# Kernel optimization log

Measured on AMD Instinct MI355X. Metric: run time of the kernel, lower is better.

Reference implementation:

```python
import jax, jax.numpy as jnp
import numpy as np

B, H, P, D = 32, 8, 16, 32
OUT_DIM = 32
GROUPS = 64
NUM_F = 8
N = H * P * D                 # 4096 (self.num)
PHO = P * H * OUT_DIM         # 4096


def setup_inputs() -> dict:
    key = jax.random.key(0)
    ks = jax.random.split(key, 10)
    return {
        "q": jax.random.normal(ks[0], (B, H, P, D), dtype=jnp.float32),
        "k": jax.random.normal(ks[1], (B, H, P, D), dtype=jnp.float32),
        "grid": jnp.arange(NUM_F, dtype=jnp.float32) + 1.0,
        "base_weight_q": jax.random.uniform(ks[2], (PHO, N), dtype=jnp.float32),
        "base_weight_k": jax.random.uniform(ks[3], (PHO, N), dtype=jnp.float32),
        "coef_q": jax.random.uniform(ks[4], (GROUPS, 1, NUM_F), dtype=jnp.float32),
        "coef_k": jax.random.uniform(ks[5], (GROUPS, 1, NUM_F), dtype=jnp.float32),
        # grouped 1x1 conv == num_f independent [PHO, N] matmuls (only conv_layer_q is used in forward)
        "conv_wq": jax.random.normal(ks[6], (NUM_F, PHO, N), dtype=jnp.float32) * 0.01,
        "conv_bq": jax.random.normal(ks[7], (NUM_F, PHO), dtype=jnp.float32) * 0.01,
        "scale_sp": jnp.ones((PHO,), dtype=jnp.float32),
    }


def reference(q, k, grid, base_weight_q, base_weight_k, coef_q, coef_k, conv_wq, conv_bq, scale_sp):
    b, h, p, d = q.shape
    n = h * p * d
    nf = grid.shape[0]
    gs = n // coef_q.shape[0]               # group_size
    out_dim = base_weight_q.shape[0] // (p * h)

    qf = q.reshape(b, n)
    kf = k.reshape(b, n)

    base_q = jax.nn.silu(qf) @ base_weight_q.T          # [B, PHO]
    base_k = jax.nn.silu(kf) @ base_weight_k.T

    # per-feature coef: feature i in group i//gs, scaled per frequency f -> [F, N]
    ce_q = jnp.repeat(coef_q[:, 0, :], gs, axis=0).T
    ce_k = jnp.repeat(coef_k[:, 0, :], gs, axis=0).T

    sq = jnp.sin(grid[None, :, None] * qf[:, None, :]) * ce_q[None]   # [B, F, N]
    sk = jnp.sin(grid[None, :, None] * kf[:, None, :]) * ce_k[None]

    # grouped conv1d (kernel 1, groups=num_f): per-frequency matmul; original uses conv_layer_q for both
    fq = jnp.einsum('bfn,fon->bfo', sq, conv_wq) + conv_bq[None]      # [B, F, PHO]
    fq = fq.sum(axis=1) * scale_sp
    fk = jnp.einsum('bfn,fon->bfo', sk, conv_wq) + conv_bq[None]
    fk = fk.sum(axis=1) * scale_sp

    y = (fq * scale_sp + base_q) + (fk * scale_sp + base_k)
    y = y.reshape(b, h, p, out_dim)
    return jax.nn.softmax(y, axis=-1)
```

## Files before the change

### kernel.cpp

```cpp
#include <hip/hip_runtime.h>
#include <math.h>

#define N_TOT 4096
#define PHO_T 4096
#define KTOT  40960
#define NS    2560

typedef __attribute__((ext_vector_type(8)))  short short8v;
typedef __attribute__((ext_vector_type(16))) float f32x16;

#define GLD16(src, dst) __builtin_amdgcn_global_load_lds(                      \
    (const __attribute__((address_space(1))) void*)(src),                      \
    (__attribute__((address_space(3))) void*)(dst), 16, 0, 0)

__device__ __forceinline__ void split1(float x, short& h, short& l) {
    unsigned u  = __builtin_bit_cast(unsigned, x);
    unsigned hu = (u + 0x7FFFu + ((u >> 16) & 1u)) & 0xFFFF0000u;
    h = (short)(hu >> 16);
    float r = x - __builtin_bit_cast(float, hu);
    unsigned ur = __builtin_bit_cast(unsigned, r);
    l = (short)((ur + 0x7FFFu + ((ur >> 16) & 1u)) >> 16);
}

__global__ void act_kernel(const float* __restrict__ q,
                           const float* __restrict__ kx,
                           const float* __restrict__ grid_,
                           const float* __restrict__ coefq,
                           const float* __restrict__ coefk,
                           short* __restrict__ Af)
{
    const int t = blockIdx.x * 256 + threadIdx.x;
    const int S = t >> 6;
    const int l = t & 63;
    const int b = l & 31;
    const int k0 = S * 16 + (l >> 5) * 8;

    float v[8];
    if (k0 < 8192) {
        const float* src = (k0 < 4096) ? (q  + (size_t)b * N_TOT + k0)
                                       : (kx + (size_t)b * N_TOT + (k0 - 4096));
#pragma unroll
        for (int j = 0; j < 8; ++j) {
            const float x = src[j];
            v[j] = x / (1.f + __expf(-x));
        }
    } else {
        const int f  = (k0 - 8192) >> 12;
        const int n0 = (k0 - 8192) & 4095;
        const int g  = n0 >> 6;
        const float gf  = grid_[f];
        const float cq_ = coefq[g * 8 + f];
        const float ck_ = coefk[g * 8 + f];
        const float* qp = q  + (size_t)b * N_TOT + n0;
        const float* kp = kx + (size_t)b * N_TOT + n0;
#pragma unroll
        for (int j = 0; j < 8; ++j)
            v[j] = __sinf(gf * qp[j]) * cq_ + __sinf(gf * kp[j]) * ck_;
    }

    short8v hi, lo;
#pragma unroll
    for (int j = 0; j < 8; ++j) { short h, lw; split1(v[j], h, lw); hi[j] = h; lo[j] = lw; }
    *(short8v*)&Af[((size_t)(S * 2 + 0) * 64 + l) * 8] = hi;
    *(short8v*)&Af[((size_t)(S * 2 + 1) * 64 + l) * 8] = lo;
}

__global__ void init_kernel(const float* __restrict__ cb,
                            const float* __restrict__ ssp,
                            float* __restrict__ ypre)
{
    const int t = blockIdx.x * 256 + threadIdx.x;
    const int o = t & 4095;
    const float s = ssp[o];
    float acc = 0.f;
#pragma unroll
    for (int f = 0; f < 8; ++f) acc += cb[f * PHO_T + o];
    ypre[t] = 2.f * s * s * acc;
}

#define OBK  256
#define KC   32
#define KSUP 1280
#define NCH  (KSUP / KC)

__global__ __launch_bounds__(256) void gemm_kernel(
    const float* __restrict__ bwq, const float* __restrict__ bwk,
    const float* __restrict__ cw,  const short* __restrict__ Af,
    const float* __restrict__ ssp, float* __restrict__ ypre)
{
    __shared__ float Wl[2][OBK * KC];

    const int t  = threadIdx.x;
    const int ks = blockIdx.x >> 4;
    const int ob = blockIdx.x & 15;
    const int o_base = ob * OBK;
    const int k_base = ks * KSUP;

    const int w  = t >> 6;
    const int l  = t & 63;
    const int srow  = l >> 3;
    const int sslot = (l & 7) ^ (srow & 7);

    f32x16 accU0, accU1, accS0, accS1;
#pragma unroll
    for (int i = 0; i < 16; ++i) {
        accU0[i] = 0.f; accU1[i] = 0.f; accS0[i] = 0.f; accS1[i] = 0.f;
    }

    auto wptr = [&](int kg) -> const float* {
        if (kg < 4096)  return bwq + kg;
        if (kg < 8192)  return bwk + (kg - 4096);
        const int f    = (kg - 8192) >> 12;
        const int noff = (kg - 8192) & 4095;
        return cw + (size_t)f * (size_t)PHO_T * N_TOT + noff;
    };

    auto stage = [&](int kg, int buf) {
        const float* Wp = wptr(kg);
#pragma unroll
        for (int i = 0; i < 8; ++i) {
            const int row = w * 64 + i * 8 + srow;
            const float* src = Wp + (size_t)(o_base + row) * N_TOT + sslot * 4;
            GLD16(src, &Wl[buf][(w * 64 + i * 8) * KC]);
        }
    };

    const int rkey = l & 7;
    const int row0 = w * 64 + (l & 31);
    const int j0b  = (l >> 5) * 2;

    auto compute = [&](int kg, int cur, const short8v& ah0, const short8v& al0,
                       const short8v& ah1, const short8v& al1) {
        const bool sc = (kg >= 8192);
#pragma unroll
        for (int s = 0; s < 2; ++s) {
            const short8v& ah = s ? ah1 : ah0;
            const short8v& al = s ? al1 : al0;
            const int j0 = s * 4 + j0b;

            auto tileop = [&](int nt, f32x16& acc) {
                const float* rp = &Wl[cur][(row0 + nt * 32) * KC];
                const float4 wa = *(const float4*)&rp[((j0    ) ^ rkey) * 4];
                const float4 wb = *(const float4*)&rp[((j0 + 1) ^ rkey) * 4];
                short8v bh, bl;
                {
                    short h, lw;
                    split1(wa.x, h, lw); bh[0] = h; bl[0] = lw;
                    split1(wa.y, h, lw); bh[1] = h; bl[1] = lw;
                    split1(wa.z, h, lw); bh[2] = h; bl[2] = lw;
                    split1(wa.w, h, lw); bh[3] = h; bl[3] = lw;
                    split1(wb.x, h, lw); bh[4] = h; bl[4] = lw;
                    split1(wb.y, h, lw); bh[5] = h; bl[5] = lw;
                    split1(wb.z, h, lw); bh[6] = h; bl[6] = lw;
                    split1(wb.w, h, lw); bh[7] = h; bl[7] = lw;
                }
                acc = __builtin_amdgcn_mfma_f32_32x32x16_bf16(ah, bh, acc, 0, 0, 0);
                acc = __builtin_amdgcn_mfma_f32_32x32x16_bf16(ah, bl, acc, 0, 0, 0);
                acc = __builtin_amdgcn_mfma_f32_32x32x16_bf16(al, bh, acc, 0, 0, 0);
            };
            if (sc) { tileop(0, accS0); tileop(1, accS1); }
            else    { tileop(0, accU0); tileop(1, accU1); }
        }
    };

    stage(k_base, 0);

    short8v ah0, al0, ah1, al1;
    for (int c = 0; c < NCH - 1; ++c) {
        const int cur = c & 1;
        const int kg  = k_base + c * KC;
        const size_t Sg = (size_t)(kg >> 4);
        ah0 = *(const short8v*)&Af[(((Sg    ) * 2 + 0) * 64 + l) * 8];
        al0 = *(const short8v*)&Af[(((Sg    ) * 2 + 1) * 64 + l) * 8];
        ah1 = *(const short8v*)&Af[(((Sg + 1) * 2 + 0) * 64 + l) * 8];
        al1 = *(const short8v*)&Af[(((Sg + 1) * 2 + 1) * 64 + l) * 8];
        asm volatile("" ::: "memory");
        stage(kg + KC, cur ^ 1);
        asm volatile("s_waitcnt vmcnt(8)" ::: "memory");
        __builtin_amdgcn_sched_barrier(0);
        compute(kg, cur, ah0, al0, ah1, al1);
    }
    {
        const int c   = NCH - 1;
        const int kg  = k_base + c * KC;
        const size_t Sg = (size_t)(kg >> 4);
        ah0 = *(const short8v*)&Af[(((Sg    ) * 2 + 0) * 64 + l) * 8];
        al0 = *(const short8v*)&Af[(((Sg    ) * 2 + 1) * 64 + l) * 8];
        ah1 = *(const short8v*)&Af[(((Sg + 1) * 2 + 0) * 64 + l) * 8];
        al1 = *(const short8v*)&Af[(((Sg + 1) * 2 + 1) * 64 + l) * 8];
        asm volatile("s_waitcnt vmcnt(0)" ::: "memory");
        __builtin_amdgcn_sched_barrier(0);
        compute(kg, c & 1, ah0, al0, ah1, al1);
    }

    const int o0 = o_base + w * 64 + (l & 31);
    const int o1 = o0 + 32;
    const float x0 = ssp[o0], x1 = ssp[o1];
    const float s0 = x0 * x0, s1 = x1 * x1;
    const int bh4 = 4 * (l >> 5);
#pragma unroll
    for (int r = 0; r < 16; ++r) {
        const int b = (r & 3) + 8 * (r >> 2) + bh4;
        atomicAdd(&ypre[(size_t)b * PHO_T + o0], accU0[r] + accS0[r] * s0);
        atomicAdd(&ypre[(size_t)b * PHO_T + o1], accU1[r] + accS1[r] * s1);
    }
}

__global__ void softmax_kernel(const float* __restrict__ yp,
                               float* __restrict__ out)
{
    const int t  = threadIdx.x;
    const int r  = blockIdx.x * 8 + (t >> 5);
    const int od = t & 31;
    const float v = yp[(size_t)r * 32 + od];
    float m = v;
#pragma unroll
    for (int s = 16; s > 0; s >>= 1) m = fmaxf(m, __shfl_xor(m, s, 32));
    const float e = __expf(v - m);
    float sum = e;
#pragma unroll
    for (int s = 16; s > 0; s >>= 1) sum += __shfl_xor(sum, s, 32);
    out[(size_t)r * 32 + od] = e / sum;
}

extern "C" void kernel_launch(void* const* d_in, const int* in_sizes, int n_in,
                              void* d_out, int out_size, void* d_ws, size_t ws_size,
                              hipStream_t stream)
{
    const float* q    = (const float*)d_in[0];
    const float* k    = (const float*)d_in[1];
    const float* grid = (const float*)d_in[2];
    const float* bwq  = (const float*)d_in[3];
    const float* bwk  = (const float*)d_in[4];
    const float* cq   = (const float*)d_in[5];
    const float* ck   = (const float*)d_in[6];
    const float* cw   = (const float*)d_in[7];
    const float* cb   = (const float*)d_in[8];
    const float* ssp  = (const float*)d_in[9];
    float* out = (float*)d_out;

    short* Af   = (short*)d_ws;
    float* ypre = (float*)((char*)d_ws + (size_t)NS * 2 * 64 * 16);

    act_kernel<<<640, 256, 0, stream>>>(q, k, grid, cq, ck, Af);
    init_kernel<<<512, 256, 0, stream>>>(cb, ssp, ypre);
    gemm_kernel<<<512, 256, 0, stream>>>(bwq, bwk, cw, Af, ssp, ypre);
    softmax_kernel<<<512, 256, 0, stream>>>(ypre, out);
}
```

Measured before the change: 142.6 us.

## Halve GEMM output tile, double grid, remap blocks, fuse init into act kernel

The output block width in the split-K GEMM drops from 256 to 128 rows, so the grid doubles from 512 to 1024 blocks and each wave keeps one accumulator pair instead of two. Block indices are remapped so that consecutive blocks share an output block while covering different K slices. The bias/init kernel is folded into the activation kernel to remove one launch. The aim is more parallelism over the 256 CUs and lower register pressure. The cost is that each A fragment is reused across fewer MFMA tiles, A-fragment global loads double, and twice as many LDS stages are issued per FLOP.

```diff
diff --git a/kernel.cpp b/kernel.cpp
--- a/kernel.cpp
+++ b/kernel.cpp
@@ -27,7 +27,10 @@
                            const float* __restrict__ grid_,
                            const float* __restrict__ coefq,
                            const float* __restrict__ coefk,
-                           short* __restrict__ Af)
+                           const float* __restrict__ cb,
+                           const float* __restrict__ ssp,
+                           short* __restrict__ Af,
+                           float* __restrict__ ypre)
 {
     const int t = blockIdx.x * 256 + threadIdx.x;
     const int S = t >> 6;
@@ -63,22 +66,18 @@
     for (int j = 0; j < 8; ++j) { short h, lw; split1(v[j], h, lw); hi[j] = h; lo[j] = lw; }
     *(short8v*)&Af[((size_t)(S * 2 + 0) * 64 + l) * 8] = hi;
     *(short8v*)&Af[((size_t)(S * 2 + 1) * 64 + l) * 8] = lo;
-}
-
-__global__ void init_kernel(const float* __restrict__ cb,
-                            const float* __restrict__ ssp,
-                            float* __restrict__ ypre)
-{
-    const int t = blockIdx.x * 256 + threadIdx.x;
-    const int o = t & 4095;
-    const float s = ssp[o];
-    float acc = 0.f;
-#pragma unroll
-    for (int f = 0; f < 8; ++f) acc += cb[f * PHO_T + o];
-    ypre[t] = 2.f * s * s * acc;
-}
-
-#define OBK  256
+
+    if (t < 32 * PHO_T) {
+        const int o = t & 4095;
+        const float s = ssp[o];
+        float acc = 0.f;
+#pragma unroll
+        for (int f = 0; f < 8; ++f) acc += cb[f * PHO_T + o];
+        ypre[t] = 2.f * s * s * acc;
+    }
+}
+
+#define OBK  128
 #define KC   32
 #define KSUP 1280
 #define NCH  (KSUP / KC)
@@ -90,9 +89,10 @@
 {
     __shared__ float Wl[2][OBK * KC];
 
-    const int t  = threadIdx.x;
-    const int ks = blockIdx.x >> 4;
-    const int ob = blockIdx.x & 15;
+    const int t   = threadIdx.x;
+    const int bid = blockIdx.x;
+    const int ks  = ((bid >> 3) & 3) * 8 + (bid & 7);
+    const int ob  = bid >> 5;
     const int o_base = ob * OBK;
     const int k_base = ks * KSUP;
 
@@ -101,11 +101,9 @@
     const int srow  = l >> 3;
     const int sslot = (l & 7) ^ (srow & 7);
 
-    f32x16 accU0, accU1, accS0, accS1;
-#pragma unroll
-    for (int i = 0; i < 16; ++i) {
-        accU0[i] = 0.f; accU1[i] = 0.f; accS0[i] = 0.f; accS1[i] = 0.f;
-    }
+    f32x16 accU, accS;
+#pragma unroll
+    for (int i = 0; i < 16; ++i) { accU[i] = 0.f; accS[i] = 0.f; }
 
     auto wptr = [&](int kg) -> const float* {
         if (kg < 4096)  return bwq + kg;
@@ -118,15 +116,15 @@
     auto stage = [&](int kg, int buf) {
         const float* Wp = wptr(kg);
 #pragma unroll
-        for (int i = 0; i < 8; ++i) {
-            const int row = w * 64 + i * 8 + srow;
+        for (int i = 0; i < 4; ++i) {
+            const int row = w * 32 + i * 8 + srow;
             const float* src = Wp + (size_t)(o_base + row) * N_TOT + sslot * 4;
-            GLD16(src, &Wl[buf][(w * 64 + i * 8) * KC]);
+            GLD16(src, &Wl[buf][(w * 32 + i * 8) * KC]);
         }
     };
 
     const int rkey = l & 7;
-    const int row0 = w * 64 + (l & 31);
+    const int row0 = w * 32 + (l & 31);
     const int j0b  = (l >> 5) * 2;
 
     auto compute = [&](int kg, int cur, const short8v& ah0, const short8v& al0,
@@ -138,28 +136,25 @@
             const short8v& al = s ? al1 : al0;
             const int j0 = s * 4 + j0b;
 
-            auto tileop = [&](int nt, f32x16& acc) {
-                const float* rp = &Wl[cur][(row0 + nt * 32) * KC];
-                const float4 wa = *(const float4*)&rp[((j0    ) ^ rkey) * 4];
-                const float4 wb = *(const float4*)&rp[((j0 + 1) ^ rkey) * 4];
-                short8v bh, bl;
-                {
-                    short h, lw;
-                    split1(wa.x, h, lw); bh[0] = h; bl[0] = lw;
-                    split1(wa.y, h, lw); bh[1] = h; bl[1] = lw;
-                    split1(wa.z, h, lw); bh[2] = h; bl[2] = lw;
-                    split1(wa.w, h, lw); bh[3] = h; bl[3] = lw;
-                    split1(wb.x, h, lw); bh[4] = h; bl[4] = lw;
-                    split1(wb.y, h, lw); bh[5] = h; bl[5] = lw;
-                    split1(wb.z, h, lw); bh[6] = h; bl[6] = lw;
-                    split1(wb.w, h, lw); bh[7] = h; bl[7] = lw;
-                }
-                acc = __builtin_amdgcn_mfma_f32_32x32x16_bf16(ah, bh, acc, 0, 0, 0);
-                acc = __builtin_amdgcn_mfma_f32_32x32x16_bf16(ah, bl, acc, 0, 0, 0);
-                acc = __builtin_amdgcn_mfma_f32_32x32x16_bf16(al, bh, acc, 0, 0, 0);
-            };
-            if (sc) { tileop(0, accS0); tileop(1, accS1); }
-            else    { tileop(0, accU0); tileop(1, accU1); }
+            const float* rp = &Wl[cur][row0 * KC];
+            const float4 wa = *(const float4*)&rp[((j0    ) ^ rkey) * 4];
+            const float4 wb = *(const float4*)&rp[((j0 + 1) ^ rkey) * 4];
+            short8v bh, bl;
+            {
+                short h, lw;
+                split1(wa.x, h, lw); bh[0] = h; bl[0] = lw;
+                split1(wa.y, h, lw); bh[1] = h; bl[1] = lw;
+                split1(wa.z, h, lw); bh[2] = h; bl[2] = lw;
+                split1(wa.w, h, lw); bh[3] = h; bl[3] = lw;
+                split1(wb.x, h, lw); bh[4] = h; bl[4] = lw;
+                split1(wb.y, h, lw); bh[5] = h; bl[5] = lw;
+                split1(wb.z, h, lw); bh[6] = h; bl[6] = lw;
+                split1(wb.w, h, lw); bh[7] = h; bl[7] = lw;
+            }
+            f32x16& acc = sc ? accS : accU;
+            acc = __builtin_amdgcn_mfma_f32_32x32x16_bf16(ah, bh, acc, 0, 0, 0);
+            acc = __builtin_amdgcn_mfma_f32_32x32x16_bf16(ah, bl, acc, 0, 0, 0);
+            acc = __builtin_amdgcn_mfma_f32_32x32x16_bf16(al, bh, acc, 0, 0, 0);
         }
     };
 
@@ -176,7 +171,7 @@
         al1 = *(const short8v*)&Af[(((Sg + 1) * 2 + 1) * 64 + l) * 8];
         asm volatile("" ::: "memory");
         stage(kg + KC, cur ^ 1);
-        asm volatile("s_waitcnt vmcnt(8)" ::: "memory");
+        asm volatile("s_waitcnt vmcnt(4)" ::: "memory");
         __builtin_amdgcn_sched_barrier(0);
         compute(kg, cur, ah0, al0, ah1, al1);
     }
@@ -193,16 +188,14 @@
         compute(kg, c & 1, ah0, al0, ah1, al1);
     }
 
-    const int o0 = o_base + w * 64 + (l & 31);
-    const int o1 = o0 + 32;
-    const float x0 = ssp[o0], x1 = ssp[o1];
-    const float s0 = x0 * x0, s1 = x1 * x1;
+    const int o0 = o_base + w * 32 + (l & 31);
+    const float x0 = ssp[o0];
+    const float s0 = x0 * x0;
     const int bh4 = 4 * (l >> 5);
 #pragma unroll
     for (int r = 0; r < 16; ++r) {
         const int b = (r & 3) + 8 * (r >> 2) + bh4;
-        atomicAdd(&ypre[(size_t)b * PHO_T + o0], accU0[r] + accS0[r] * s0);
-        atomicAdd(&ypre[(size_t)b * PHO_T + o1], accU1[r] + accS1[r] * s1);
+        atomicAdd(&ypre[(size_t)b * PHO_T + o0], accU[r] + accS[r] * s0);
     }
 }
 
@@ -242,8 +235,7 @@
     short* Af   = (short*)d_ws;
     float* ypre = (float*)((char*)d_ws + (size_t)NS * 2 * 64 * 16);
 
-    act_kernel<<<640, 256, 0, stream>>>(q, k, grid, cq, ck, Af);
-    init_kernel<<<512, 256, 0, stream>>>(cb, ssp, ypre);
-    gemm_kernel<<<512, 256, 0, stream>>>(bwq, bwk, cw, Af, ssp, ypre);
+    act_kernel<<<640, 256, 0, stream>>>(q, k, grid, cq, ck, cb, ssp, Af, ypre);
+    gemm_kernel<<<1024, 256, 0, stream>>>(bwq, bwk, cw, Af, ssp, ypre);
     softmax_kernel<<<512, 256, 0, stream>>>(ypre, out);
 }
```

Measured after the change: 150.7 us. 1.06x slower.

## Replace split-K atomics with partial buffers and fuse reduction, bias and softmax

Applied to the files above, without the earlier changes.

The GEMM kernel now writes its split-K partial sums to per-slice buffers with plain stores instead of atomicAdd into a pre-initialised output. A new kernel sums the 32 partials, adds the conv bias term and applies the softmax, replacing both the init kernel and the separate softmax kernel. This removes atomic contention and one launch. In exchange it needs a 16 MB partial-sum workspace and a reduction pass that reads it back.

```diff
diff --git a/kernel.cpp b/kernel.cpp
--- a/kernel.cpp
+++ b/kernel.cpp
@@ -5,6 +5,7 @@
 #define PHO_T 4096
 #define KTOT  40960
 #define NS    2560
+#define NSUP  32
 
 typedef __attribute__((ext_vector_type(8)))  short short8v;
 typedef __attribute__((ext_vector_type(16))) float f32x16;
@@ -65,19 +66,6 @@
     *(short8v*)&Af[((size_t)(S * 2 + 1) * 64 + l) * 8] = lo;
 }
 
-__global__ void init_kernel(const float* __restrict__ cb,
-                            const float* __restrict__ ssp,
-                            float* __restrict__ ypre)
-{
-    const int t = blockIdx.x * 256 + threadIdx.x;
-    const int o = t & 4095;
-    const float s = ssp[o];
-    float acc = 0.f;
-#pragma unroll
-    for (int f = 0; f < 8; ++f) acc += cb[f * PHO_T + o];
-    ypre[t] = 2.f * s * s * acc;
-}
-
 #define OBK  256
 #define KC   32
 #define KSUP 1280
@@ -86,7 +74,7 @@
 __global__ __launch_bounds__(256) void gemm_kernel(
     const float* __restrict__ bwq, const float* __restrict__ bwk,
     const float* __restrict__ cw,  const short* __restrict__ Af,
-    const float* __restrict__ ssp, float* __restrict__ ypre)
+    const float* __restrict__ ssp, float* __restrict__ ypart)
 {
     __shared__ float Wl[2][OBK * KC];
 
@@ -193,6 +181,7 @@
         compute(kg, c & 1, ah0, al0, ah1, al1);
     }
 
+    float* __restrict__ yp = ypart + (size_t)ks * (32 * PHO_T);
     const int o0 = o_base + w * 64 + (l & 31);
     const int o1 = o0 + 32;
     const float x0 = ssp[o0], x1 = ssp[o1];
@@ -201,26 +190,38 @@
 #pragma unroll
     for (int r = 0; r < 16; ++r) {
         const int b = (r & 3) + 8 * (r >> 2) + bh4;
-        atomicAdd(&ypre[(size_t)b * PHO_T + o0], accU0[r] + accS0[r] * s0);
-        atomicAdd(&ypre[(size_t)b * PHO_T + o1], accU1[r] + accS1[r] * s1);
-    }
-}
-
-__global__ void softmax_kernel(const float* __restrict__ yp,
-                               float* __restrict__ out)
-{
-    const int t  = threadIdx.x;
-    const int r  = blockIdx.x * 8 + (t >> 5);
-    const int od = t & 31;
-    const float v = yp[(size_t)r * 32 + od];
+        yp[(size_t)b * PHO_T + o0] = accU0[r] + accS0[r] * s0;
+        yp[(size_t)b * PHO_T + o1] = accU1[r] + accS1[r] * s1;
+    }
+}
+
+__global__ void reduce_softmax_kernel(const float* __restrict__ ypart,
+                                      const float* __restrict__ cb,
+                                      const float* __restrict__ ssp,
+                                      float* __restrict__ out)
+{
+    const int e = blockIdx.x * 256 + threadIdx.x;
+    const int o = e & 4095;
+
+    float v = 0.f;
+#pragma unroll
+    for (int ks = 0; ks < NSUP; ++ks)
+        v += ypart[(size_t)ks * (32 * PHO_T) + e];
+
+    float bias = 0.f;
+#pragma unroll
+    for (int f = 0; f < 8; ++f) bias += cb[f * PHO_T + o];
+    const float ss = ssp[o];
+    v += 2.f * ss * ss * bias;
+
     float m = v;
 #pragma unroll
     for (int s = 16; s > 0; s >>= 1) m = fmaxf(m, __shfl_xor(m, s, 32));
-    const float e = __expf(v - m);
-    float sum = e;
+    const float ex = __expf(v - m);
+    float sum = ex;
 #pragma unroll
     for (int s = 16; s > 0; s >>= 1) sum += __shfl_xor(sum, s, 32);
-    out[(size_t)r * 32 + od] = e / sum;
+    out[e] = ex / sum;
 }
 
 extern "C" void kernel_launch(void* const* d_in, const int* in_sizes, int n_in,
@@ -239,11 +240,10 @@
     const float* ssp  = (const float*)d_in[9];
     float* out = (float*)d_out;
 
-    short* Af   = (short*)d_ws;
-    float* ypre = (float*)((char*)d_ws + (size_t)NS * 2 * 64 * 16);
+    short* Af    = (short*)d_ws;
+    float* ypart = (float*)((char*)d_ws + (size_t)NS * 2 * 64 * 16);
 
     act_kernel<<<640, 256, 0, stream>>>(q, k, grid, cq, ck, Af);
-    init_kernel<<<512, 256, 0, stream>>>(cb, ssp, ypre);
-    gemm_kernel<<<512, 256, 0, stream>>>(bwq, bwk, cw, Af, ssp, ypre);
-    softmax_kernel<<<512, 256, 0, stream>>>(ypre, out);
-}
+    gemm_kernel<<<512, 256, 0, stream>>>(bwq, bwk, cw, Af, ssp, ypart);
+    reduce_softmax_kernel<<<512, 256, 0, stream>>>(ypart, cb, ssp, out);
+}
```

New measurement: 141.3 us. About the same (-0.9%).
